# Kernel tuning notes

Measured on AMD Instinct MI355X. Metric: run time of the kernel, lower is better.

## Reference

```python
import jax, jax.numpy as jnp
import numpy as np

N, D, DB, E, H = 1024, 512, 64, 32768, 1024

def setup_inputs() -> dict:
    key = jax.random.key(0)
    k = jax.random.split(key, 6)
    object_feats = jax.random.normal(k[0], (N, D), dtype=jnp.float32)
    bboxes_embedding = jax.random.normal(k[1], (N, N, DB), dtype=jnp.float32)
    pairs = jax.random.randint(k[2], (E, 2), 0, N, dtype=jnp.int64)
    # Kaiming-normal-ish init for the two Linear layers
    W1 = jax.random.normal(k[3], (D + D + DB, H), dtype=jnp.float32) * np.sqrt(2.0 / (D + D + DB))
    b1 = jnp.zeros((H,), dtype=jnp.float32)
    W2 = jax.random.normal(k[4], (H, D), dtype=jnp.float32) * np.sqrt(2.0 / H)
    b2 = jnp.zeros((D,), dtype=jnp.float32)
    return {"object_feats": object_feats, "bboxes_embedding": bboxes_embedding,
            "pairs": pairs, "W1": W1, "b1": b1, "W2": W2, "b2": b2}

def reference(object_feats, bboxes_embedding, pairs, W1, b1, W2, b2):
    sub = pairs[:, 0]
    obj = pairs[:, 1]
    # gather pair features: [E, D] each, plus pairwise bbox embedding [E, DB]
    f_sub = object_feats[sub]
    f_obj = object_feats[obj]
    bb = bboxes_embedding[sub, obj]
    x = jnp.concatenate((f_sub, f_obj, bb), axis=1)  # [E, 2D+DB]
    h = jax.nn.relu(x @ W1 + b1)
    out = h @ W2 + b2  # [E, D]
    n = object_feats.shape[0]
    # scatter-mean into subject nodes; each node's own feature is included once,
    # so new_feat[i] = (object_feats[i] + sum_{pairs with sub==i} out) / (1 + count[i]).
    # Nodes with no incident pairs keep their original feature (count==0 -> identity).
    seg_sum = jax.ops.segment_sum(out, sub, num_segments=n)  # [N, D]
    count = jax.ops.segment_sum(jnp.ones((out.shape[0],), dtype=out.dtype), sub, num_segments=n)
    new_feats = (object_feats + seg_sum) / (1.0 + count)[:, None]
    return (new_feats, bboxes_embedding, pairs)
```

## Files before the change

### kernel.cpp

```cpp
#include <hip/hip_runtime.h>

#define N_OBJ 1024
#define E_P   32768

typedef float f32x4 __attribute__((ext_vector_type(4)));
typedef short bf16x8 __attribute__((ext_vector_type(8)));
typedef unsigned short u16x4 __attribute__((ext_vector_type(4)));

__device__ __forceinline__ unsigned short f2bf(float f) {
    unsigned u = __float_as_uint(f);
    u = u + 0x7FFFu + ((u >> 16) & 1u);
    return (unsigned short)(u >> 16);
}

#define OFF_A    0
#define LEN_A    3670016
#define OFF_B    (OFF_A + LEN_A)
#define LEN_B    3145728
#define OFF_SEG  (OFF_B + LEN_B)
#define LEN_SEG  6815744
#define OFF_OUT  (OFF_SEG + LEN_SEG)
#define LEN_OUT  3145728

__device__ __forceinline__ void copy_nt(const f32x4* __restrict__ src,
                                        f32x4* __restrict__ dst,
                                        int off, int len, int nb, int cb) {
    int stride = nb * 256;
    int i = off + cb * 256 + threadIdx.x;
    int end = off + len;
    for (; i + stride < end; i += 2 * stride) {
        f32x4 a = __builtin_nontemporal_load(&src[i]);
        f32x4 b = __builtin_nontemporal_load(&src[i + stride]);
        __builtin_nontemporal_store(a, &dst[i]);
        __builtin_nontemporal_store(b, &dst[i + stride]);
    }
    if (i < end) {
        f32x4 a = __builtin_nontemporal_load(&src[i]);
        __builtin_nontemporal_store(a, &dst[i]);
    }
}

__global__ __launch_bounds__(256) void k_zero(int* __restrict__ counts) {
    ((int4*)counts)[threadIdx.x] = make_int4(0, 0, 0, 0);
}

__global__ __launch_bounds__(256) void k_zero_hs(float4* __restrict__ hs4) {
    int i = blockIdx.x * 256 + threadIdx.x;
    const int stride = 256 * 256;
    float4 z = make_float4(0.f, 0.f, 0.f, 0.f);
    #pragma unroll
    for (int it = 0; it < 4; ++it) { hs4[i] = z; i += stride; }
}

__global__ __launch_bounds__(256) void k_a(const float* __restrict__ W1,
                                           const float* __restrict__ W2,
                                           const float* __restrict__ feats,
                                           const int* __restrict__ pairs,
                                           const float* __restrict__ bb,
                                           unsigned short* __restrict__ w1pqT,
                                           unsigned short* __restrict__ w1cT,
                                           unsigned short* __restrict__ w2T,
                                           unsigned short* __restrict__ featsb,
                                           float* __restrict__ out_pairs,
                                           int* __restrict__ counts,
                                           int* __restrict__ rank,
                                           float* __restrict__ bbg,
                                           const f32x4* __restrict__ csrc,
                                           f32x4* __restrict__ cdst) {
    int bid = blockIdx.x, tid = threadIdx.x;
    if ((bid % 3) == 2) { copy_nt(csrc, cdst, OFF_A, LEN_A, 1184, bid / 3); return; }
    int job = (bid / 3) * 2 + (bid % 3);
    if (job >= 2240) return;
    if (job >= 2112) {
        int e = (job - 2112) * 256 + tid;
        int sub = pairs[2 * e], obj = pairs[2 * e + 1];
        const f32x4* src = (const f32x4*)&bb[((size_t)sub * 1024 + (size_t)obj) * 64];
        f32x4* dst = (f32x4*)&bbg[(size_t)e * 64];
        #pragma unroll
        for (int i = 0; i < 16; ++i) {
            f32x4 v = __builtin_nontemporal_load(&src[i]);
            dst[i] = v;
        }
        return;
    }
    if (job >= 1856) {
        int i = (job - 1856) * 256 + tid;
        out_pairs[i] = (float)pairs[i];
        if (i < E_P) rank[i] = atomicAdd(&counts[pairs[2 * i]], 1);
        return;
    }
    if (job >= 1600) {
        int base = (job - 1600) * 2048 + tid * 8;
        float4 v0 = *(const float4*)&feats[base];
        float4 v1 = *(const float4*)&feats[base + 4];
        u16x4 o0 = { f2bf(v0.x), f2bf(v0.y), f2bf(v0.z), f2bf(v0.w) };
        u16x4 o1 = { f2bf(v1.x), f2bf(v1.y), f2bf(v1.z), f2bf(v1.w) };
        *(u16x4*)&featsb[base] = o0;
        *(u16x4*)&featsb[base + 4] = o1;
        return;
    }
    const float* in; unsigned short* out;
    int LDI, LDO, r0, c0, nbase, kbase;
    if (job < 1024) {
        r0 = (job >> 5) * 32; c0 = (job & 31) * 32;
        in = W1; LDI = 1024; out = w1pqT; LDO = 512;
        nbase = c0 + (r0 >= 512 ? 1024 : 0); kbase = r0 & 511;
    } else if (job < 1088) {
        int t = job - 1024; r0 = 1024 + (t >> 5) * 32; c0 = (t & 31) * 32;
        in = W1; LDI = 1024; out = w1cT; LDO = 64;
        nbase = c0; kbase = r0 - 1024;
    } else {
        int t = job - 1088; r0 = (t >> 4) * 32; c0 = (t & 15) * 32;
        in = W2; LDI = 512; out = w2T; LDO = 1024;
        nbase = c0; kbase = r0;
    }
    __shared__ float lds[32][33];
    int ti = tid >> 3, tj = (tid & 7) * 4;
    float4 v = *(const float4*)&in[(size_t)(r0 + ti) * LDI + c0 + tj];
    lds[ti][tj] = v.x; lds[ti][tj + 1] = v.y; lds[ti][tj + 2] = v.z; lds[ti][tj + 3] = v.w;
    __syncthreads();
    int oc = tid >> 3, oj = (tid & 7) * 4;
    u16x4 o = { f2bf(lds[oj][oc]), f2bf(lds[oj + 1][oc]),
                f2bf(lds[oj + 2][oc]), f2bf(lds[oj + 3][oc]) };
    *(u16x4*)&out[(size_t)(nbase + oc) * LDO + kbase + oj] = o;
}

__global__ __launch_bounds__(256) void k_b(const int* __restrict__ counts,
                                           const int* __restrict__ rank,
                                           const int* __restrict__ pairs,
                                           int* __restrict__ csr_obj,
                                           int* __restrict__ csr_e,
                                           unsigned* __restrict__ brec,
                                           int* __restrict__ bcnt,
                                           const unsigned short* __restrict__ featsb,
                                           const unsigned short* __restrict__ w1pqT,
                                           const float* __restrict__ b1,
                                           float* __restrict__ P, float* __restrict__ Q,
                                           const f32x4* __restrict__ csrc,
                                           f32x4* __restrict__ cdst) {
    int bid = blockIdx.x, tid = threadIdx.x;
    if ((bid % 3) < 2) { copy_nt(csrc, cdst, OFF_B, LEN_B, 1282, (bid / 3) * 2 + (bid % 3)); return; }
    int role = bid / 3;

    if (role >= 129) {
        int job = role - 129;
        int m0 = (job >> 5) * 64, n0 = (job & 31) * 64;
        int w = tid >> 6, l = tid & 63;
        int ln = l & 15, kb = (l >> 4) * 8;
        int row = m0 + w * 16 + ln;
        f32x4 acc[4] = {};
        for (int k0 = 0; k0 < 512; k0 += 32) {
            bf16x8 a = *(const bf16x8*)&featsb[(size_t)row * 512 + k0 + kb];
            #pragma unroll
            for (int f = 0; f < 4; ++f) {
                bf16x8 b = *(const bf16x8*)&w1pqT[(size_t)(n0 + f * 16 + ln) * 512 + k0 + kb];
                acc[f] = __builtin_amdgcn_mfma_f32_16x16x32_bf16(a, b, acc[f], 0, 0, 0);
            }
        }
        int mr = m0 + w * 16 + (l >> 4) * 4;
        if (n0 < 1024) {
            #pragma unroll
            for (int f = 0; f < 4; ++f) {
                int n = n0 + f * 16 + ln;
                float b1v = b1[n];
                #pragma unroll
                for (int r = 0; r < 4; ++r)
                    P[(size_t)(mr + r) * 1024 + n] = acc[f][r] + b1v;
            }
        } else {
            #pragma unroll
            for (int f = 0; f < 4; ++f) {
                int n = n0 - 1024 + f * 16 + ln;
                #pragma unroll
                for (int r = 0; r < 4; ++r)
                    Q[(size_t)(mr + r) * 1024 + n] = acc[f][r];
            }
        }
        return;
    }

    __shared__ int sbuf[2][256];
    __shared__ int soff[1024];
    int c[4]; int s = 0;
    #pragma unroll
    for (int i = 0; i < 4; ++i) { c[i] = counts[tid * 4 + i]; s += c[i]; }
    sbuf[0][tid] = s;
    __syncthreads();
    int sel = 0;
    for (int d = 1; d < 256; d <<= 1) {
        int v = sbuf[sel][tid];
        if (tid >= d) v += sbuf[sel][tid - d];
        sbuf[sel ^ 1][tid] = v;
        sel ^= 1;
        __syncthreads();
    }
    int base = sbuf[sel][tid] - s;
    int run = base;
    #pragma unroll
    for (int i = 0; i < 4; ++i) { soff[tid * 4 + i] = run; run += c[i]; }
    __syncthreads();

    if (role >= 1) {
        int e = (role - 1) * 256 + tid;
        int sub = pairs[2 * e];
        int pos = soff[sub] + rank[e];
        csr_obj[pos] = pairs[2 * e + 1];
        csr_e[pos] = e;
        return;
    }

    int nb[4]; int t = 0;
    #pragma unroll
    for (int i = 0; i < 4; ++i) { nb[i] = (c[i] + 31) >> 5; t += nb[i]; }
    __syncthreads();
    sbuf[0][tid] = t;
    __syncthreads();
    sel = 0;
    for (int d = 1; d < 256; d <<= 1) {
        int v = sbuf[sel][tid];
        if (tid >= d) v += sbuf[sel][tid - d];
        sbuf[sel ^ 1][tid] = v;
        sel ^= 1;
        __syncthreads();
    }
    int bpos = sbuf[sel][tid] - t;
    int run2 = base;
    #pragma unroll
    for (int i = 0; i < 4; ++i) {
        int seg = tid * 4 + i;
        for (int k = 0; k < nb[i]; ++k) {
            int st = run2 + k * 32;
            int cnt = c[i] - k * 32; if (cnt > 32) cnt = 32;
            brec[bpos++] = (unsigned)st | ((unsigned)seg << 16) | ((unsigned)(cnt - 1) << 26);
        }
        run2 += c[i];
    }
    if (tid == 255) bcnt[0] = bpos;
}

__global__ __launch_bounds__(256) void k_seg(const int* __restrict__ csr_obj,
                                             const int* __restrict__ csr_e,
                                             const unsigned* __restrict__ brec,
                                             const int* __restrict__ bcnt,
                                             const float* __restrict__ bbg,
                                             const unsigned short* __restrict__ w1cT,
                                             const float* __restrict__ P,
                                             const float* __restrict__ Q,
                                             float* __restrict__ HS,
                                             const f32x4* __restrict__ csrc,
                                             f32x4* __restrict__ cdst) {
    int bid = blockIdx.x;
    if ((bid % 5) == 4) { copy_nt(csrc, cdst, OFF_SEG, LEN_SEG, 2048, bid / 5); return; }
    int job = (bid / 5) * 4 + (bid % 5);
    int b = job >> 2, qd = job & 3;
    if (b >= bcnt[0]) return;
    unsigned rec = brec[b];
    const int start = rec & 0xFFFF;
    const int seg = (rec >> 16) & 0x3FF;
    const int n = ((rec >> 26) & 31) + 1;

    const int tid = threadIdx.x, w = tid >> 6, l = tid & 63;
    const int ln = l & 15, g4 = l >> 4, kb = g4 * 8;
    const int cbase = qd * 256;
    const int wbase = cbase + w * 64;

    __shared__ float qs[32][256];

    {
        int p = tid >> 3, j = tid & 7;
        int op = csr_obj[start + (p < n ? p : n - 1)];
        const float* qrow = &Q[(size_t)op * 1024 + cbase];
        #pragma unroll
        for (int i = 0; i < 8; ++i) {
            int c = j * 4 + i * 32;
            *(float4*)&qs[p][c] = *(const float4*)&qrow[c];
        }
    }

    const int nA = n < 16 ? n : 16;
    const int nB = n - 16;
    int iA = start + (ln < nA ? ln : nA - 1);
    int iB = (nB > 0) ? (start + 16 + (ln < nB ? ln : nB - 1)) : iA;
    int eA = csr_e[iA];
    int eB = csr_e[iB];

    const float* brA = &bbg[(size_t)eA * 64];
    const float* brB = &bbg[(size_t)eB * 64];
    float4 a0 = *(const float4*)&brA[kb];
    float4 a1 = *(const float4*)&brA[kb + 4];
    float4 a2 = *(const float4*)&brA[32 + kb];
    float4 a3 = *(const float4*)&brA[32 + kb + 4];
    float4 c0 = *(const float4*)&brB[kb];
    float4 c1 = *(const float4*)&brB[kb + 4];
    float4 c2 = *(const float4*)&brB[32 + kb];
    float4 c3 = *(const float4*)&brB[32 + kb + 4];
    bf16x8 A0a, A1a, A0b, A1b;
    A0a[0] = (short)f2bf(a0.x); A0a[1] = (short)f2bf(a0.y); A0a[2] = (short)f2bf(a0.z); A0a[3] = (short)f2bf(a0.w);
    A0a[4] = (short)f2bf(a1.x); A0a[5] = (short)f2bf(a1.y); A0a[6] = (short)f2bf(a1.z); A0a[7] = (short)f2bf(a1.w);
    A1a[0] = (short)f2bf(a2.x); A1a[1] = (short)f2bf(a2.y); A1a[2] = (short)f2bf(a2.z); A1a[3] = (short)f2bf(a2.w);
    A1a[4] = (short)f2bf(a3.x); A1a[5] = (short)f2bf(a3.y); A1a[6] = (short)f2bf(a3.z); A1a[7] = (short)f2bf(a3.w);
    A0b[0] = (short)f2bf(c0.x); A0b[1] = (short)f2bf(c0.y); A0b[2] = (short)f2bf(c0.z); A0b[3] = (short)f2bf(c0.w);
    A0b[4] = (short)f2bf(c1.x); A0b[5] = (short)f2bf(c1.y); A0b[6] = (short)f2bf(c1.z); A0b[7] = (short)f2bf(c1.w);
    A1b[0] = (short)f2bf(c2.x); A1b[1] = (short)f2bf(c2.y); A1b[2] = (short)f2bf(c2.z); A1b[3] = (short)f2bf(c2.w);
    A1b[4] = (short)f2bf(c3.x); A1b[5] = (short)f2bf(c3.y); A1b[6] = (short)f2bf(c3.z); A1b[7] = (short)f2bf(c3.w);

    bool vA0 = (g4 * 4 + 0) < nA, vA1 = (g4 * 4 + 1) < nA;
    bool vA2 = (g4 * 4 + 2) < nA, vA3 = (g4 * 4 + 3) < nA;
    bool vB0 = (g4 * 4 + 0) < nB, vB1 = (g4 * 4 + 1) < nB;
    bool vB2 = (g4 * 4 + 2) < nB, vB3 = (g4 * 4 + 3) < nB;

    float pv[4];
    #pragma unroll
    for (int f = 0; f < 4; ++f)
        pv[f] = P[(size_t)seg * 1024 + wbase + f * 16 + ln];

    __syncthreads();

    #pragma unroll
    for (int f = 0; f < 4; ++f) {
        int col = wbase + f * 16 + ln;
        int cc = col - cbase;
        const unsigned short* wr = &w1cT[(size_t)col * 64];
        bf16x8 b0 = *(const bf16x8*)&wr[kb];
        bf16x8 b1 = *(const bf16x8*)&wr[32 + kb];
        f32x4 dA = {0.f, 0.f, 0.f, 0.f};
        dA = __builtin_amdgcn_mfma_f32_16x16x32_bf16(A0a, b0, dA, 0, 0, 0);
        dA = __builtin_amdgcn_mfma_f32_16x16x32_bf16(A1a, b1, dA, 0, 0, 0);
        f32x4 dB = {0.f, 0.f, 0.f, 0.f};
        dB = __builtin_amdgcn_mfma_f32_16x16x32_bf16(A0b, b0, dB, 0, 0, 0);
        dB = __builtin_amdgcn_mfma_f32_16x16x32_bf16(A1b, b1, dB, 0, 0, 0);
        float qA0 = qs[g4 * 4 + 0][cc];
        float qA1 = qs[g4 * 4 + 1][cc];
        float qA2 = qs[g4 * 4 + 2][cc];
        float qA3 = qs[g4 * 4 + 3][cc];
        float qB0 = qs[16 + g4 * 4 + 0][cc];
        float qB1 = qs[16 + g4 * 4 + 1][cc];
        float qB2 = qs[16 + g4 * 4 + 2][cc];
        float qB3 = qs[16 + g4 * 4 + 3][cc];
        float h = 0.f;
        h += vA0 ? fmaxf(dA[0] + pv[f] + qA0, 0.f) : 0.f;
        h += vA1 ? fmaxf(dA[1] + pv[f] + qA1, 0.f) : 0.f;
        h += vA2 ? fmaxf(dA[2] + pv[f] + qA2, 0.f) : 0.f;
        h += vA3 ? fmaxf(dA[3] + pv[f] + qA3, 0.f) : 0.f;
        h += vB0 ? fmaxf(dB[0] + pv[f] + qB0, 0.f) : 0.f;
        h += vB1 ? fmaxf(dB[1] + pv[f] + qB1, 0.f) : 0.f;
        h += vB2 ? fmaxf(dB[2] + pv[f] + qB2, 0.f) : 0.f;
        h += vB3 ? fmaxf(dB[3] + pv[f] + qB3, 0.f) : 0.f;
        h += __shfl_xor(h, 16);
        h += __shfl_xor(h, 32);
        if (l < 16) atomicAdd(&HS[(size_t)seg * 1024 + wbase + f * 16 + l], h);
    }
}

__global__ __launch_bounds__(256) void k_out(const float* __restrict__ HS,
                                             const unsigned short* __restrict__ w2T,
                                             const float* __restrict__ feats,
                                             const float* __restrict__ b2,
                                             const int* __restrict__ counts,
                                             float* __restrict__ out0,
                                             const f32x4* __restrict__ csrc,
                                             f32x4* __restrict__ cdst) {
    int bid = blockIdx.x;
    if ((bid % 17) != 16) { copy_nt(csrc, cdst, OFF_OUT, LEN_OUT, 2048, (bid / 17) * 16 + (bid % 17)); return; }
    int job = bid / 17;
    int m0 = (job >> 3) * 64, n0 = (job & 7) * 64;
    int tid = threadIdx.x, w = tid >> 6, l = tid & 63;
    int ln = l & 15, kb = (l >> 4) * 8;
    int row = m0 + w * 16 + ln;
    f32x4 acc[4] = {};
    for (int k0 = 0; k0 < 1024; k0 += 32) {
        const float* hp = &HS[(size_t)row * 1024 + k0 + kb];
        float4 h0 = *(const float4*)&hp[0];
        float4 h1 = *(const float4*)&hp[4];
        bf16x8 a;
        a[0] = (short)f2bf(h0.x); a[1] = (short)f2bf(h0.y); a[2] = (short)f2bf(h0.z); a[3] = (short)f2bf(h0.w);
        a[4] = (short)f2bf(h1.x); a[5] = (short)f2bf(h1.y); a[6] = (short)f2bf(h1.z); a[7] = (short)f2bf(h1.w);
        #pragma unroll
        for (int f = 0; f < 4; ++f) {
            bf16x8 b = *(const bf16x8*)&w2T[(size_t)(n0 + f * 16 + ln) * 1024 + k0 + kb];
            acc[f] = __builtin_amdgcn_mfma_f32_16x16x32_bf16(a, b, acc[f], 0, 0, 0);
        }
    }
    int mr = m0 + w * 16 + (l >> 4) * 4;
    float cv[4], inv[4];
    #pragma unroll
    for (int r = 0; r < 4; ++r) {
        float c = (float)counts[mr + r];
        cv[r] = c;
        inv[r] = 1.0f / (1.0f + c);
    }
    #pragma unroll
    for (int f = 0; f < 4; ++f) {
        int n = n0 + f * 16 + ln;
        float b2v = b2[n];
        #pragma unroll
        for (int r = 0; r < 4; ++r) {
            float fv = feats[(size_t)(mr + r) * 512 + n];
            out0[(size_t)(mr + r) * 512 + n] = (fv + acc[f][r] + cv[r] * b2v) * inv[r];
        }
    }
}

extern "C" void kernel_launch(void* const* d_in, const int* in_sizes, int n_in,
                              void* d_out, int out_size, void* d_ws, size_t ws_size,
                              hipStream_t stream) {
    const float* feats = (const float*)d_in[0];
    const float* bb    = (const float*)d_in[1];
    const int*   pairs = (const int*)d_in[2];
    const float* W1    = (const float*)d_in[3];
    const float* b1    = (const float*)d_in[4];
    const float* W2    = (const float*)d_in[5];
    const float* b2    = (const float*)d_in[6];

    float* out        = (float*)d_out;
    float* out_feats  = out;
    float* out_bb     = out + (size_t)N_OBJ * 512;
    float* out_pairs  = out + (size_t)N_OBJ * 512 + (size_t)N_OBJ * N_OBJ * 64;

    char* w = (char*)d_ws;
    unsigned short* featsb = (unsigned short*)w;
    unsigned short* w1pqT  = (unsigned short*)(w + (1u << 20));
    float*          HS     = (float*)w;
    unsigned short* w1cT   = (unsigned short*)(w + (4u << 20));
    unsigned short* w2T    = (unsigned short*)(w + (4u << 20) + (128u << 10));
    float* P = (float*)(w + (5u << 20) + (128u << 10));
    float* Q = (float*)(w + (9u << 20) + (128u << 10));
    char* ints = w + (13u << 20) + (128u << 10);
    int*      counts  = (int*)ints;
    int*      csr_obj = (int*)(ints + 4096);
    unsigned* brec    = (unsigned*)(ints + 4096 + 131072);
    int*      bcnt    = (int*)(ints + 4096 + 131072 + 16384);
    int*      rank    = (int*)(ints + 4096 + 131072 + 16384 + 64);
    int*      csr_e   = (int*)(ints + 4096 + 131072 + 16384 + 64 + 131072);
    float*    bbg     = (float*)(w + (14u << 20));

    const f32x4* cbb  = (const f32x4*)bb;
    f32x4*       cobb = (f32x4*)out_bb;

    k_zero<<<1, 256, 0, stream>>>(counts);

    k_a<<<3552, 256, 0, stream>>>(W1, W2, feats, pairs, bb, w1pqT, w1cT, w2T, featsb,
                                  out_pairs, counts, rank, bbg, cbb, cobb);
    k_b<<<1923, 256, 0, stream>>>(counts, rank, pairs, csr_obj, csr_e, brec, bcnt,
                                  featsb, w1pqT, b1, P, Q, cbb, cobb);

    k_zero_hs<<<256, 256, 0, stream>>>((float4*)HS);

    k_seg<<<10240, 256, 0, stream>>>(csr_obj, csr_e, brec, bcnt, bbg, w1cT, P, Q, HS,
                                     cbb, cobb);
    k_out<<<2176, 256, 0, stream>>>(HS, w2T, feats, b2, counts, out_feats, cbb, cobb);
}
```

Baseline: 235.1 us.

## Store gathered bbox rows and Q in bf16, fold HS zeroing into k_a

Gathered bbox embeddings and the Q projection are now written as bf16 instead of fp32. This halves their write and read traffic and removes the per-element conversion in the segment kernel. HS zeroing moves into spare blocks of k_a, which drops one kernel launch, and the workspace is relaid so HS no longer aliases featsb. The bulk bbox copy is rebalanced across kernels, with more copy work placed in k_a and k_b and less in k_seg, and k_seg gets a new block-to-job mapping. Q rounded to bf16 adds a small precision loss to the pre-activation sum.

```diff
diff --git a/kernel.cpp b/kernel.cpp
--- a/kernel.cpp
+++ b/kernel.cpp
@@ -12,13 +12,16 @@
     u = u + 0x7FFFu + ((u >> 16) & 1u);
     return (unsigned short)(u >> 16);
 }
+__device__ __forceinline__ float bf2f(unsigned short u) {
+    return __uint_as_float(((unsigned)u) << 16);
+}
 
 #define OFF_A    0
-#define LEN_A    3670016
+#define LEN_A    5242880
 #define OFF_B    (OFF_A + LEN_A)
-#define LEN_B    3145728
+#define LEN_B    4194304
 #define OFF_SEG  (OFF_B + LEN_B)
-#define LEN_SEG  6815744
+#define LEN_SEG  4194304
 #define OFF_OUT  (OFF_SEG + LEN_SEG)
 #define LEN_OUT  3145728
 
@@ -42,14 +45,6 @@
 
 __global__ __launch_bounds__(256) void k_zero(int* __restrict__ counts) {
     ((int4*)counts)[threadIdx.x] = make_int4(0, 0, 0, 0);
-}
-
-__global__ __launch_bounds__(256) void k_zero_hs(float4* __restrict__ hs4) {
-    int i = blockIdx.x * 256 + threadIdx.x;
-    const int stride = 256 * 256;
-    float4 z = make_float4(0.f, 0.f, 0.f, 0.f);
-    #pragma unroll
-    for (int it = 0; it < 4; ++it) { hs4[i] = z; i += stride; }
 }
 
 __global__ __launch_bounds__(256) void k_a(const float* __restrict__ W1,
@@ -64,22 +59,31 @@
                                            float* __restrict__ out_pairs,
                                            int* __restrict__ counts,
                                            int* __restrict__ rank,
-                                           float* __restrict__ bbg,
+                                           unsigned short* __restrict__ bbgb,
+                                           f32x4* __restrict__ hs4,
                                            const f32x4* __restrict__ csrc,
                                            f32x4* __restrict__ cdst) {
     int bid = blockIdx.x, tid = threadIdx.x;
-    if ((bid % 3) == 2) { copy_nt(csrc, cdst, OFF_A, LEN_A, 1184, bid / 3); return; }
+    if ((bid % 3) == 2) { copy_nt(csrc, cdst, OFF_A, LEN_A, 1152, bid / 3); return; }
     int job = (bid / 3) * 2 + (bid % 3);
-    if (job >= 2240) return;
+    if (job >= 2240) {
+        int blk = job - 2240;
+        f32x4 z = {0.f, 0.f, 0.f, 0.f};
+        f32x4* p = hs4 + (size_t)blk * 4096 + tid;
+        #pragma unroll
+        for (int it = 0; it < 16; ++it) p[it * 256] = z;
+        return;
+    }
     if (job >= 2112) {
         int e = (job - 2112) * 256 + tid;
         int sub = pairs[2 * e], obj = pairs[2 * e + 1];
         const f32x4* src = (const f32x4*)&bb[((size_t)sub * 1024 + (size_t)obj) * 64];
-        f32x4* dst = (f32x4*)&bbg[(size_t)e * 64];
+        u16x4* dst = (u16x4*)&bbgb[(size_t)e * 64];
         #pragma unroll
         for (int i = 0; i < 16; ++i) {
             f32x4 v = __builtin_nontemporal_load(&src[i]);
-            dst[i] = v;
+            u16x4 o = { f2bf(v.x), f2bf(v.y), f2bf(v.z), f2bf(v.w) };
+            dst[i] = o;
         }
         return;
     }
@@ -135,7 +139,8 @@
                                            const unsigned short* __restrict__ featsb,
                                            const unsigned short* __restrict__ w1pqT,
                                            const float* __restrict__ b1,
-                                           float* __restrict__ P, float* __restrict__ Q,
+                                           float* __restrict__ P,
+                                           unsigned short* __restrict__ Qb,
                                            const f32x4* __restrict__ csrc,
                                            f32x4* __restrict__ cdst) {
     int bid = blockIdx.x, tid = threadIdx.x;
@@ -173,7 +178,7 @@
                 int n = n0 - 1024 + f * 16 + ln;
                 #pragma unroll
                 for (int r = 0; r < 4; ++r)
-                    Q[(size_t)(mr + r) * 1024 + n] = acc[f][r];
+                    Qb[(size_t)(mr + r) * 1024 + n] = f2bf(acc[f][r]);
             }
         }
         return;
@@ -242,38 +247,41 @@
                                              const int* __restrict__ csr_e,
                                              const unsigned* __restrict__ brec,
                                              const int* __restrict__ bcnt,
-                                             const float* __restrict__ bbg,
+                                             const unsigned short* __restrict__ bbgb,
                                              const unsigned short* __restrict__ w1cT,
                                              const float* __restrict__ P,
-                                             const float* __restrict__ Q,
+                                             const unsigned short* __restrict__ Qb,
                                              float* __restrict__ HS,
                                              const f32x4* __restrict__ csrc,
                                              f32x4* __restrict__ cdst) {
-    int bid = blockIdx.x;
-    if ((bid % 5) == 4) { copy_nt(csrc, cdst, OFF_SEG, LEN_SEG, 2048, bid / 5); return; }
-    int job = (bid / 5) * 4 + (bid % 5);
-    int b = job >> 2, qd = job & 3;
+    int bid = blockIdx.x, tid = threadIdx.x;
+    int x = bid & 7, k = bid >> 3;
+    if (k >= 1024) { copy_nt(csrc, cdst, OFF_SEG, LEN_SEG, 4096, (k - 1024) * 8 + x); return; }
+    int qd = x >> 1;
+    int b = k * 2 + (x & 1);
     if (b >= bcnt[0]) return;
     unsigned rec = brec[b];
     const int start = rec & 0xFFFF;
     const int seg = (rec >> 16) & 0x3FF;
     const int n = ((rec >> 26) & 31) + 1;
 
-    const int tid = threadIdx.x, w = tid >> 6, l = tid & 63;
+    const int w = tid >> 6, l = tid & 63;
     const int ln = l & 15, g4 = l >> 4, kb = g4 * 8;
     const int cbase = qd * 256;
     const int wbase = cbase + w * 64;
 
-    __shared__ float qs[32][256];
+    __shared__ unsigned short qs[32][264];
 
     {
         int p = tid >> 3, j = tid & 7;
-        int op = csr_obj[start + (p < n ? p : n - 1)];
-        const float* qrow = &Q[(size_t)op * 1024 + cbase];
-        #pragma unroll
-        for (int i = 0; i < 8; ++i) {
-            int c = j * 4 + i * 32;
-            *(float4*)&qs[p][c] = *(const float4*)&qrow[c];
+        if (p < n) {
+            int op = csr_obj[start + p];
+            const uint4* qrow = (const uint4*)&Qb[(size_t)op * 1024 + cbase];
+            #pragma unroll
+            for (int i = 0; i < 4; ++i) {
+                uint4 v = qrow[j * 4 + i];
+                *(uint4*)&qs[p][(j * 4 + i) * 8] = v;
+            }
         }
     }
 
@@ -284,25 +292,12 @@
     int eA = csr_e[iA];
     int eB = csr_e[iB];
 
-    const float* brA = &bbg[(size_t)eA * 64];
-    const float* brB = &bbg[(size_t)eB * 64];
-    float4 a0 = *(const float4*)&brA[kb];
-    float4 a1 = *(const float4*)&brA[kb + 4];
-    float4 a2 = *(const float4*)&brA[32 + kb];
-    float4 a3 = *(const float4*)&brA[32 + kb + 4];
-    float4 c0 = *(const float4*)&brB[kb];
-    float4 c1 = *(const float4*)&brB[kb + 4];
-    float4 c2 = *(const float4*)&brB[32 + kb];
-    float4 c3 = *(const float4*)&brB[32 + kb + 4];
-    bf16x8 A0a, A1a, A0b, A1b;
-    A0a[0] = (short)f2bf(a0.x); A0a[1] = (short)f2bf(a0.y); A0a[2] = (short)f2bf(a0.z); A0a[3] = (short)f2bf(a0.w);
-    A0a[4] = (short)f2bf(a1.x); A0a[5] = (short)f2bf(a1.y); A0a[6] = (short)f2bf(a1.z); A0a[7] = (short)f2bf(a1.w);
-    A1a[0] = (short)f2bf(a2.x); A1a[1] = (short)f2bf(a2.y); A1a[2] = (short)f2bf(a2.z); A1a[3] = (short)f2bf(a2.w);
-    A1a[4] = (short)f2bf(a3.x); A1a[5] = (short)f2bf(a3.y); A1a[6] = (short)f2bf(a3.z); A1a[7] = (short)f2bf(a3.w);
-    A0b[0] = (short)f2bf(c0.x); A0b[1] = (short)f2bf(c0.y); A0b[2] = (short)f2bf(c0.z); A0b[3] = (short)f2bf(c0.w);
-    A0b[4] = (short)f2bf(c1.x); A0b[5] = (short)f2bf(c1.y); A0b[6] = (short)f2bf(c1.z); A0b[7] = (short)f2bf(c1.w);
-    A1b[0] = (short)f2bf(c2.x); A1b[1] = (short)f2bf(c2.y); A1b[2] = (short)f2bf(c2.z); A1b[3] = (short)f2bf(c2.w);
-    A1b[4] = (short)f2bf(c3.x); A1b[5] = (short)f2bf(c3.y); A1b[6] = (short)f2bf(c3.z); A1b[7] = (short)f2bf(c3.w);
+    const unsigned short* brA = &bbgb[(size_t)eA * 64];
+    const unsigned short* brB = &bbgb[(size_t)eB * 64];
+    bf16x8 A0a = *(const bf16x8*)&brA[kb];
+    bf16x8 A1a = *(const bf16x8*)&brA[32 + kb];
+    bf16x8 A0b = *(const bf16x8*)&brB[kb];
+    bf16x8 A1b = *(const bf16x8*)&brB[32 + kb];
 
     bool vA0 = (g4 * 4 + 0) < nA, vA1 = (g4 * 4 + 1) < nA;
     bool vA2 = (g4 * 4 + 2) < nA, vA3 = (g4 * 4 + 3) < nA;
@@ -329,14 +324,14 @@
         f32x4 dB = {0.f, 0.f, 0.f, 0.f};
         dB = __builtin_amdgcn_mfma_f32_16x16x32_bf16(A0b, b0, dB, 0, 0, 0);
         dB = __builtin_amdgcn_mfma_f32_16x16x32_bf16(A1b, b1, dB, 0, 0, 0);
-        float qA0 = qs[g4 * 4 + 0][cc];
-        float qA1 = qs[g4 * 4 + 1][cc];
-        float qA2 = qs[g4 * 4 + 2][cc];
-        float qA3 = qs[g4 * 4 + 3][cc];
-        float qB0 = qs[16 + g4 * 4 + 0][cc];
-        float qB1 = qs[16 + g4 * 4 + 1][cc];
-        float qB2 = qs[16 + g4 * 4 + 2][cc];
-        float qB3 = qs[16 + g4 * 4 + 3][cc];
+        float qA0 = bf2f(qs[g4 * 4 + 0][cc]);
+        float qA1 = bf2f(qs[g4 * 4 + 1][cc]);
+        float qA2 = bf2f(qs[g4 * 4 + 2][cc]);
+        float qA3 = bf2f(qs[g4 * 4 + 3][cc]);
+        float qB0 = bf2f(qs[16 + g4 * 4 + 0][cc]);
+        float qB1 = bf2f(qs[16 + g4 * 4 + 1][cc]);
+        float qB2 = bf2f(qs[16 + g4 * 4 + 2][cc]);
+        float qB3 = bf2f(qs[16 + g4 * 4 + 3][cc]);
         float h = 0.f;
         h += vA0 ? fmaxf(dA[0] + pv[f] + qA0, 0.f) : 0.f;
         h += vA1 ? fmaxf(dA[1] + pv[f] + qA1, 0.f) : 0.f;
@@ -420,33 +415,30 @@
     char* w = (char*)d_ws;
     unsigned short* featsb = (unsigned short*)w;
     unsigned short* w1pqT  = (unsigned short*)(w + (1u << 20));
-    float*          HS     = (float*)w;
-    unsigned short* w1cT   = (unsigned short*)(w + (4u << 20));
-    unsigned short* w2T    = (unsigned short*)(w + (4u << 20) + (128u << 10));
-    float* P = (float*)(w + (5u << 20) + (128u << 10));
-    float* Q = (float*)(w + (9u << 20) + (128u << 10));
-    char* ints = w + (13u << 20) + (128u << 10);
+    unsigned short* w1cT   = (unsigned short*)(w + (3u << 20));
+    unsigned short* w2T    = (unsigned short*)(w + (3u << 20) + (128u << 10));
+    float*          HS     = (float*)(w + (4u << 20) + (128u << 10));
+    float*          P      = (float*)(w + (8u << 20) + (128u << 10));
+    unsigned short* Qb     = (unsigned short*)(w + (12u << 20) + (128u << 10));
+    unsigned short* bbgb   = (unsigned short*)(w + (14u << 20) + (128u << 10));
+    char* ints = w + (18u << 20) + (128u << 10);
     int*      counts  = (int*)ints;
     int*      csr_obj = (int*)(ints + 4096);
-    unsigned* brec    = (unsigned*)(ints + 4096 + 131072);
-    int*      bcnt    = (int*)(ints + 4096 + 131072 + 16384);
-    int*      rank    = (int*)(ints + 4096 + 131072 + 16384 + 64);
-    int*      csr_e   = (int*)(ints + 4096 + 131072 + 16384 + 64 + 131072);
-    float*    bbg     = (float*)(w + (14u << 20));
+    int*      csr_e   = (int*)(ints + 4096 + 131072);
+    unsigned* brec    = (unsigned*)(ints + 4096 + 262144);
+    int*      bcnt    = (int*)(ints + 4096 + 262144 + 16384);
+    int*      rank    = (int*)(ints + 4096 + 262144 + 16384 + 64);
 
     const f32x4* cbb  = (const f32x4*)bb;
     f32x4*       cobb = (f32x4*)out_bb;
 
     k_zero<<<1, 256, 0, stream>>>(counts);
 
-    k_a<<<3552, 256, 0, stream>>>(W1, W2, feats, pairs, bb, w1pqT, w1cT, w2T, featsb,
-                                  out_pairs, counts, rank, bbg, cbb, cobb);
+    k_a<<<3456, 256, 0, stream>>>(W1, W2, feats, pairs, bb, w1pqT, w1cT, w2T, featsb,
+                                  out_pairs, counts, rank, bbgb, (f32x4*)HS, cbb, cobb);
     k_b<<<1923, 256, 0, stream>>>(counts, rank, pairs, csr_obj, csr_e, brec, bcnt,
-                                  featsb, w1pqT, b1, P, Q, cbb, cobb);
-
-    k_zero_hs<<<256, 256, 0, stream>>>((float4*)HS);
-
-    k_seg<<<10240, 256, 0, stream>>>(csr_obj, csr_e, brec, bcnt, bbg, w1cT, P, Q, HS,
+                                  featsb, w1pqT, b1, P, Qb, cbb, cobb);
+    k_seg<<<12288, 256, 0, stream>>>(csr_obj, csr_e, brec, bcnt, bbgb, w1cT, P, Qb, HS,
                                      cbb, cobb);
     k_out<<<2176, 256, 0, stream>>>(HS, w2T, feats, b2, counts, out_feats, cbb, cobb);
 }
```

New measurement: 218.6 us. -7.0%, faster.
